# Optimization experiments

Hardware: AMD Instinct MI355X
Metric: run time of the kernel (lower is better)

## Reference

```python
import jax, jax.numpy as jnp
import numpy as np

T, B, I, H, L = 512, 32, 1024, 1024, 2


def setup_inputs() -> dict:
    key = jax.random.key(0)
    ks = jax.random.split(key, 10)
    stdv = 1.0 / np.sqrt(H)
    u = lambda k, shape: jax.random.uniform(k, shape, jnp.float32, -stdv, stdv)
    return {
        "x": jax.random.normal(ks[0], (T, B, I), jnp.float32),
        "h0": jnp.zeros((L, B, H), jnp.float32),
        "c0": jnp.zeros((L, B, H), jnp.float32),
        "W0": u(ks[1], (4 * H, I)),
        "R0": u(ks[2], (4 * H, H)),
        "bi0": u(ks[3], (4 * H,)),
        "bh0": u(ks[4], (4 * H,)),
        "W1": u(ks[5], (4 * H, H)),
        "R1": u(ks[6], (4 * H, H)),
        "bi1": u(ks[7], (4 * H,)),
        "bh1": u(ks[8], (4 * H,)),
    }


def _run_layer(x, h_init, c_init, W, R, bi, bh):
    # Precompute input projection for all timesteps: [T, B, 4H]
    xg = jnp.einsum('tbi,gi->tbg', x, W) + bi

    def step(carry, xg_t):
        h, c = carry
        gates = jax.nn.sigmoid(xg_t + h @ R.T + bh)  # [B, 4H]
        i_g, o_g, z_g, f_g = jnp.split(gates, 4, axis=-1)
        c = c * f_g + z_g - i_g          # subtractive cell update
        h = jax.nn.sigmoid(c) - o_g      # subtractive output
        return (h, c), h

    (hT, cT), out = jax.lax.scan(step, (h_init, c_init), xg)
    return out, hT, cT


def reference(x, h0, c0, W0, R0, bi0, bh0, W1, R1, bi1, bh1):
    layers = [(W0, R0, bi0, bh0), (W1, R1, bi1, bh1)]
    out = x
    h_finals, c_finals = [], []
    for l, (W, R, bi, bh) in enumerate(layers):
        out, hT, cT = _run_layer(out, h0[l], c0[l], W, R, bi, bh)
        h_finals.append(hT)
        c_finals.append(cT)
    return out, (jnp.stack(h_finals), jnp.stack(c_finals))
```

## Files before the change

### kernel.cpp

```cpp
#include <hip/hip_runtime.h>

typedef unsigned short ushort_t;
typedef unsigned int uint_t;
typedef __bf16 bf16x8 __attribute__((ext_vector_type(8)));
typedef float f32x4 __attribute__((ext_vector_type(4)));

#define T_STEPS 512
#define NWG 256

union bfu { uint4 u; bf16x8 v; };

__device__ __forceinline__ float bf2f(ushort_t u) {
  union { unsigned u; float f; } v; v.u = ((unsigned)u) << 16; return v.f;
}
__device__ __forceinline__ ushort_t f2bf(float f) {
  union { float f; unsigned u; } v; v.f = f;
  unsigned r = (v.u + 0x7FFFu + ((v.u >> 16) & 1u)) >> 16;
  return (ushort_t)r;
}
__device__ __forceinline__ uint_t pack2(float a, float b) {
  return (uint_t)f2bf(a) | ((uint_t)f2bf(b) << 16);
}
__device__ __forceinline__ float sigf(float x) {
  return 1.0f / (1.0f + __expf(-x));
}

__global__ void __launch_bounds__(256) cvt_f32_bf16(
    const float* __restrict__ in, ushort_t* __restrict__ outp, int n4) {
  int i = blockIdx.x * 256 + threadIdx.x;
  const int stride = gridDim.x * 256;
  for (; i < n4; i += stride) {
    float4 v = ((const float4*)in)[i];
    ushort4 o;
    o.x = f2bf(v.x); o.y = f2bf(v.y); o.z = f2bf(v.z); o.w = f2bf(v.w);
    ((ushort4*)outp)[i] = o;
  }
}

__global__ void __launch_bounds__(256) init_h(
    const float* __restrict__ h0_all, ushort_t* __restrict__ hpp0,
    ushort_t* __restrict__ hpp1) {
  int i = blockIdx.x * 256 + threadIdx.x;
  int l = i >> 13, j = i & 8191;
  float4 v = ((const float4*)(h0_all + l * 32768))[j];
  ushort4 o;
  o.x = f2bf(v.x); o.y = f2bf(v.y); o.z = f2bf(v.z); o.w = f2bf(v.w);
  ((ushort4*)((l ? hpp1 : hpp0) + 32768))[j] = o;
}

__global__ void __launch_bounds__(256, 1) gemm_xg(
    const float* __restrict__ X, const ushort_t* __restrict__ Wm,
    const float* __restrict__ bi, ushort_t* __restrict__ outp) {
  __shared__ char smem[65536];
  const int tid = threadIdx.x;
  const int lane = tid & 63, w = tid >> 6;
  const int m0 = blockIdx.x * 128, n0 = blockIdx.y * 128;
  const int wr = w >> 1, wc = w & 1;
  const int lr = lane & 15, kg = lane >> 4;
  const int ar_ = tid & 127;
  const int abq = (tid >> 7) * 4;

  f32x4 acc[4][4] = {};
  float4 fa[8];

  auto stageA_issue = [&](int kt) {
    const float* src = X + (size_t)(m0 + ar_) * 1024 + kt * 64 + abq * 8;
#pragma unroll
    for (int i = 0; i < 4; ++i) {
      fa[2 * i] = *(const float4*)(src + i * 8);
      fa[2 * i + 1] = *(const float4*)(src + i * 8 + 4);
    }
  };
  auto stageA_write = [&](int p) {
    char* sA = smem + p * 32768;
#pragma unroll
    for (int i = 0; i < 4; ++i) {
      int blk = abq + i;
      uint4 o;
      o.x = pack2(fa[2 * i].x, fa[2 * i].y);
      o.y = pack2(fa[2 * i].z, fa[2 * i].w);
      o.z = pack2(fa[2 * i + 1].x, fa[2 * i + 1].y);
      o.w = pack2(fa[2 * i + 1].z, fa[2 * i + 1].w);
      *(uint4*)(sA + ar_ * 128 + ((blk ^ (ar_ & 7)) << 4)) = o;
    }
  };
  auto stageB = [&](int kt, int p) {
    const int ks = kt * 64;
    char* sB = smem + p * 32768 + 16384;
#pragma unroll
    for (int i = 0; i < 4; ++i) {
      int wi = w * 4 + i;
      int e = wi * 64 + lane;
      int row = e >> 3, pb = e & 7;
      int kb = pb ^ (row & 7);
      const ushort_t* gB = Wm + (size_t)(n0 + row) * 1024 + ks + kb * 8;
      __builtin_amdgcn_global_load_lds(
          (const __attribute__((address_space(1))) void*)gB,
          (__attribute__((address_space(3))) void*)(sB + wi * 1024), 16, 0, 0);
    }
  };

  stageA_issue(0);
  stageB(0, 0);
  stageA_write(0);
  __syncthreads();
#pragma unroll 1
  for (int kt = 0; kt < 16; ++kt) {
    const int p = kt & 1;
    if (kt < 15) { stageA_issue(kt + 1); stageB(kt + 1, p ^ 1); }
    const char* sA = smem + p * 32768;
    const char* sB = sA + 16384;
#pragma unroll
    for (int k2 = 0; k2 < 2; ++k2) {
      bf16x8 af[4], bf[4];
#pragma unroll
      for (int mt = 0; mt < 4; ++mt) {
        int ar = wr * 64 + mt * 16 + lr;
        int kb = k2 * 4 + kg;
        af[mt] = *(const bf16x8*)(sA + ar * 128 + ((kb ^ (ar & 7)) << 4));
      }
#pragma unroll
      for (int nt = 0; nt < 4; ++nt) {
        int br = wc * 64 + nt * 16 + lr;
        int kb = k2 * 4 + kg;
        bf[nt] = *(const bf16x8*)(sB + br * 128 + ((kb ^ (br & 7)) << 4));
      }
#pragma unroll
      for (int mt = 0; mt < 4; ++mt)
#pragma unroll
        for (int nt = 0; nt < 4; ++nt)
          acc[mt][nt] = __builtin_amdgcn_mfma_f32_16x16x32_bf16(
              af[mt], bf[nt], acc[mt][nt], 0, 0, 0);
    }
    if (kt < 15) stageA_write(p ^ 1);
    __syncthreads();
  }
#pragma unroll
  for (int nt = 0; nt < 4; ++nt) {
    int gc = n0 + wc * 64 + nt * 16 + lr;
    int pc = ((gc & 1023) >> 3) * 32 + (gc & 7) * 4 + (gc >> 10);
    float bv = bi[gc];
#pragma unroll
    for (int mt = 0; mt < 4; ++mt) {
#pragma unroll
      for (int r = 0; r < 4; ++r) {
        int gr = m0 + wr * 64 + mt * 16 + kg * 4 + r;
        outp[(size_t)gr * 4096 + pc] = f2bf(acc[mt][nt][r] + bv);
      }
    }
  }
}

#define GLD4(dst, addr)                                        \
  asm volatile("global_load_dwordx4 %0, %1, off sc0 sc1"      \
               : "=v"(dst) : "v"(addr))
#define WAITN(N)                                               \
  do {                                                         \
    asm volatile("s_waitcnt vmcnt(" #N ")" ::: "memory");      \
    __builtin_amdgcn_sched_barrier(0);                         \
  } while (0)

__global__ void __launch_bounds__(512, 1) fused_rec(
    const ushort_t* __restrict__ xg0p, const float* __restrict__ R0,
    const float* __restrict__ R1, const float* __restrict__ W1,
    const float* __restrict__ bh0, const float* __restrict__ bi1,
    const float* __restrict__ bh1, const float* __restrict__ c0_all,
    float* __restrict__ out_f, float* __restrict__ hfinb,
    float* __restrict__ cfinb, ushort_t* __restrict__ hpp0,
    ushort_t* __restrict__ hpp1, uint_t* __restrict__ flags) {
  extern __shared__ char smem[];
  char* hl = smem;
  float* gl = (float*)(smem + 131072);

  const int tid = threadIdx.x;
  const int wg = blockIdx.x;
  const int layer = wg >> 7;
  const int wgl = wg & 127;
  const int j0 = wgl * 8;
  const int lane = tid & 63, w = tid >> 6;
  const int n16 = (w & 1) << 4;
  const int kq = w >> 1;
  const int lr16 = lane & 15, kg = lane >> 4;
  const int b = (tid >> 3) & 31, jj = tid & 7;
  const int rx = lr16 & 7;

  const int c = n16 + lr16;
  const int r_w = ((c >> 3) << 10) + j0 + (c & 7);
  bf16x8 breg[16];
  if (layer == 0) {
#pragma unroll
    for (int i = 0; i < 8; ++i) {
      const float* src = R0 + (size_t)r_w * 1024 + kq * 256 + i * 32 + kg * 8;
      float4 f0 = *(const float4*)src;
      float4 f1 = *(const float4*)(src + 4);
      bfu o;
      o.u.x = pack2(f0.x, f0.y); o.u.y = pack2(f0.z, f0.w);
      o.u.z = pack2(f1.x, f1.y); o.u.w = pack2(f1.z, f1.w);
      breg[i] = o.v;
    }
  } else {
#pragma unroll
    for (int i = 0; i < 16; ++i) {
      int k = kq * 512 + i * 32 + kg * 8;
      const float* src = (k < 1024) ? (R1 + (size_t)r_w * 1024 + k)
                                    : (W1 + (size_t)r_w * 1024 + (k - 1024));
      float4 f0 = *(const float4*)src;
      float4 f1 = *(const float4*)(src + 4);
      bfu o;
      o.u.x = pack2(f0.x, f0.y); o.u.y = pack2(f0.z, f0.w);
      o.u.z = pack2(f1.x, f1.y); o.u.w = pack2(f1.z, f1.w);
      breg[i] = o.v;
    }
  }

  float bhv[4];
#pragma unroll
  for (int g = 0; g < 4; ++g) {
    int gi = g * 1024 + j0 + jj;
    bhv[g] = layer ? (bi1[gi] + bh1[gi]) : bh0[gi];
  }
  const int cidx = b * 1024 + j0 + jj;
  float c_st = c0_all[layer * 32768 + cidx];
  uint_t* hppd = (uint_t*)(layer ? hpp1 : hpp0);
  __syncthreads();

#pragma unroll 1
  for (int s = 0; s <= T_STEPS; ++s) {
    const bool active = layer ? (s >= 1) : (s < T_STEPS);
    if (active) {
      const int t = layer ? (s - 1) : s;
      uint2 xgu = {0, 0};
      uint4 hv[16];
      if (layer == 0) {
        const char* xga = (const char*)xg0p +
            (((size_t)t * 32 + b) * 4096 + wgl * 32 + jj * 4) * 2;
        asm volatile("global_load_dwordx2 %0, %1, off"
                     : "=v"(xgu) : "v"(xga));
        const char* hsrc =
            (const char*)hpp0 + (((t + 1) & 1) << 16) + tid * 16;
#pragma unroll
        for (int l = 0; l < 8; ++l) GLD4(hv[l], hsrc + l * 8192);
        WAITN(0);
#pragma unroll
        for (int l = 0; l < 8; ++l) {
          int idx = l * 512 + tid;
          int row = idx >> 7, kb = idx & 127;
          *(uint4*)(hl + row * 2048 + ((kb ^ (row & 7)) << 4)) = hv[l];
        }
      } else {
        const char* h1src =
            (const char*)hpp1 + (((t + 1) & 1) << 16) + tid * 16;
        const char* h0src =
            (const char*)hpp0 + ((t & 1) << 16) + tid * 16;
#pragma unroll
        for (int l = 0; l < 8; ++l) GLD4(hv[l], h1src + l * 8192);
#pragma unroll
        for (int l = 0; l < 8; ++l) GLD4(hv[8 + l], h0src + l * 8192);
        WAITN(8);
#pragma unroll
        for (int l = 0; l < 8; ++l) {
          int idx = l * 512 + tid;
          int row = idx >> 7, kb = idx & 127;
          *(uint4*)(hl + row * 2048 + ((kb ^ (row & 7)) << 4)) = hv[l];
        }
        WAITN(0);
#pragma unroll
        for (int l = 0; l < 8; ++l) {
          int idx = l * 512 + tid;
          int row = idx >> 7, kb = idx & 127;
          *(uint4*)(hl + 65536 + row * 2048 + ((kb ^ (row & 7)) << 4)) =
              hv[8 + l];
        }
      }
      __syncthreads();

      f32x4 acc0 = {0.f, 0.f, 0.f, 0.f}, acc1 = {0.f, 0.f, 0.f, 0.f};
      if (layer == 0) {
        const char* a0 = hl + lr16 * 2048;
        const char* a1 = hl + (16 + lr16) * 2048;
#pragma unroll
        for (int i = 0; i < 8; ++i) {
          int kb = kq * 32 + i * 4 + kg;
          bf16x8 av0 = *(const bf16x8*)(a0 + ((kb ^ rx) << 4));
          bf16x8 av1 = *(const bf16x8*)(a1 + ((kb ^ rx) << 4));
          acc0 = __builtin_amdgcn_mfma_f32_16x16x32_bf16(av0, breg[i], acc0,
                                                         0, 0, 0);
          acc1 = __builtin_amdgcn_mfma_f32_16x16x32_bf16(av1, breg[i], acc1,
                                                         0, 0, 0);
        }
      } else {
        const char* buf = hl + ((kq >> 1) ? 65536 : 0);
        const char* a0 = buf + lr16 * 2048;
        const char* a1 = buf + (16 + lr16) * 2048;
#pragma unroll
        for (int i = 0; i < 16; ++i) {
          int kb = (kq & 1) * 64 + i * 4 + kg;
          bf16x8 av0 = *(const bf16x8*)(a0 + ((kb ^ rx) << 4));
          bf16x8 av1 = *(const bf16x8*)(a1 + ((kb ^ rx) << 4));
          acc0 = __builtin_amdgcn_mfma_f32_16x16x32_bf16(av0, breg[i], acc0,
                                                         0, 0, 0);
          acc1 = __builtin_amdgcn_mfma_f32_16x16x32_bf16(av1, breg[i], acc1,
                                                         0, 0, 0);
        }
      }
#pragma unroll
      for (int r = 0; r < 4; ++r) {
        gl[(kq * 32 + kg * 4 + r) * 33 + n16 + lr16] = acc0[r];
        gl[(kq * 32 + 16 + kg * 4 + r) * 33 + n16 + lr16] = acc1[r];
      }
      __syncthreads();

      if (tid < 256) {
        float pre[4];
#pragma unroll
        for (int g = 0; g < 4; ++g) {
          int col = g * 8 + jj;
          pre[g] = gl[(0 * 32 + b) * 33 + col] + gl[(1 * 32 + b) * 33 + col] +
                   gl[(2 * 32 + b) * 33 + col] + gl[(3 * 32 + b) * 33 + col] +
                   bhv[g];
        }
        if (layer == 0) {
          pre[0] += bf2f((ushort_t)(xgu.x & 0xffff));
          pre[1] += bf2f((ushort_t)(xgu.x >> 16));
          pre[2] += bf2f((ushort_t)(xgu.y & 0xffff));
          pre[3] += bf2f((ushort_t)(xgu.y >> 16));
        }
        float ig = sigf(pre[0]), og = sigf(pre[1]);
        float zg = sigf(pre[2]), fg = sigf(pre[3]);
        c_st = c_st * fg + zg - ig;
        float hv_ = sigf(c_st) - og;
        if (layer) out_f[(size_t)t * 32768 + cidx] = hv_;

        ushort_t hb = f2bf(hv_);
        int partner = __shfl_down((int)hb, 1, 64);
        if ((tid & 1) == 0) {
          uint_t packed =
              (uint_t)hb | (((uint_t)(unsigned short)partner) << 16);
          uint_t* dst = hppd + (((t & 1) << 14) + (cidx >> 1));
          asm volatile("global_store_dword %0, %1, off sc0 sc1"
                       :: "v"(dst), "v"(packed) : "memory");
        }
        if (t == T_STEPS - 1) {
          hfinb[layer * 32768 + cidx] = hv_;
          cfinb[layer * 32768 + cidx] = c_st;
        }
      }
    }
    if (s < T_STEPS) {
      const uint_t gen1 = (uint_t)s + 1u;
      asm volatile("s_waitcnt vmcnt(0)" ::: "memory");
      __syncthreads();
      if (tid == 0)
        __hip_atomic_store(&flags[wg], gen1, __ATOMIC_RELAXED,
                           __HIP_MEMORY_SCOPE_AGENT);
      if (tid < NWG) {
        while (__hip_atomic_load(&flags[tid], __ATOMIC_RELAXED,
                                 __HIP_MEMORY_SCOPE_AGENT) < gen1) {
          __builtin_amdgcn_s_sleep(1);
        }
      }
      __syncthreads();
      asm volatile("" ::: "memory");
    }
  }
}

extern "C" void kernel_launch(void* const* d_in, const int* in_sizes, int n_in,
                              void* d_out, int out_size, void* d_ws,
                              size_t ws_size, hipStream_t stream) {
  (void)in_sizes; (void)n_in; (void)out_size; (void)ws_size;
  const float* x = (const float*)d_in[0];
  const float* h0 = (const float*)d_in[1];
  const float* c0 = (const float*)d_in[2];
  const float* W0 = (const float*)d_in[3];
  const float* R0 = (const float*)d_in[4];
  const float* bi0 = (const float*)d_in[5];
  const float* bh0 = (const float*)d_in[6];
  const float* W1 = (const float*)d_in[7];
  const float* R1 = (const float*)d_in[8];
  const float* bi1 = (const float*)d_in[9];
  const float* bh1 = (const float*)d_in[10];
  float* outp = (float*)d_out;

  char* ws = (char*)d_ws;
  ushort_t* Wbf0 = (ushort_t*)ws;
  ushort_t* xg0p = (ushort_t*)(ws + 8388608);
  ushort_t* hpp0 = (ushort_t*)(ws + 8388608 + 134217728);
  ushort_t* hpp1 = (ushort_t*)((char*)hpp0 + 131072);
  uint_t* flags = (uint_t*)((char*)hpp1 + 131072);

  const int REC_LDS = 131072 + 4 * 32 * 33 * 4;
  (void)hipFuncSetAttribute((const void*)fused_rec,
                            hipFuncAttributeMaxDynamicSharedMemorySize,
                            REC_LDS);
  (void)hipMemsetAsync(flags, 0, NWG * sizeof(uint_t), stream);

  float* hfinb = outp + 16777216;
  float* cfinb = hfinb + 65536;

  cvt_f32_bf16<<<dim3(1024), dim3(256), 0, stream>>>(W0, Wbf0, 1048576);
  init_h<<<dim3(64), dim3(256), 0, stream>>>(h0, hpp0, hpp1);
  gemm_xg<<<dim3(128, 32), dim3(256), 0, stream>>>(x, Wbf0, bi0, xg0p);
  fused_rec<<<dim3(NWG), dim3(512), REC_LDS, stream>>>(
      xg0p, R0, R1, W1, bh0, bi1, bh1, c0, outp, hfinb, cfinb,
      hpp0, hpp1, flags);
}
```

Baseline: 4.598 ms.

## Replace global all-WG barrier with per-layer flag waits and 4-deep h0 ring

Swaps the single grid-wide barrier per step for split flags: each layer waits on its own 128 workgroups for the current step and on the other layer only for the dependency it needs. Layer 1 waits for layer 0 step t, and layer 0 may run up to three steps ahead of layer 1. To allow that slack, layer 0's hidden-state buffer becomes a 4-slot ring and the xg load is prefetched one step ahead. This removes lockstep coupling between the layers and the cross-layer skew wait, at the cost of more complex ring indexing and more memory-ordering risk.

```diff
diff --git a/kernel.cpp b/kernel.cpp
--- a/kernel.cpp
+++ b/kernel.cpp
@@ -45,7 +45,7 @@
   float4 v = ((const float4*)(h0_all + l * 32768))[j];
   ushort4 o;
   o.x = f2bf(v.x); o.y = f2bf(v.y); o.z = f2bf(v.z); o.w = f2bf(v.w);
-  ((ushort4*)((l ? hpp1 : hpp0) + 32768))[j] = o;
+  ((ushort4*)(l ? (hpp1 + 32768) : (hpp0 + 98304)))[j] = o;
 }
 
 __global__ void __launch_bounds__(256, 1) gemm_xg(
@@ -167,7 +167,8 @@
     const float* __restrict__ bh1, const float* __restrict__ c0_all,
     float* __restrict__ out_f, float* __restrict__ hfinb,
     float* __restrict__ cfinb, ushort_t* __restrict__ hpp0,
-    ushort_t* __restrict__ hpp1, uint_t* __restrict__ flags) {
+    ushort_t* __restrict__ hpp1, uint_t* __restrict__ flags0,
+    uint_t* __restrict__ flags1) {
   extern __shared__ char smem[];
   char* hl = smem;
   float* gl = (float*)(smem + 131072);
@@ -184,6 +185,9 @@
   const int b = (tid >> 3) & 31, jj = tid & 7;
   const int rx = lr16 & 7;
 
+  uint_t* fown = layer ? flags1 : flags0;
+  uint_t* foth = layer ? flags0 : flags1;
+
   const int c = n16 + lr16;
   const int r_w = ((c >> 3) << 10) + j0 + (c & 7);
   bf16x8 breg[16];
@@ -222,146 +226,154 @@
   const int cidx = b * 1024 + j0 + jj;
   float c_st = c0_all[layer * 32768 + cidx];
   uint_t* hppd = (uint_t*)(layer ? hpp1 : hpp0);
+
+  const char* xgbase = (const char*)xg0p +
+      ((size_t)b * 4096 + (size_t)wgl * 32 + (size_t)jj * 4) * 2;
+  uint2 xgu = {0, 0}, xgn = {0, 0};
+  if (layer == 0)
+    asm volatile("global_load_dwordx2 %0, %1, off" : "=v"(xgu) : "v"(xgbase));
   __syncthreads();
 
 #pragma unroll 1
-  for (int s = 0; s <= T_STEPS; ++s) {
-    const bool active = layer ? (s >= 1) : (s < T_STEPS);
-    if (active) {
-      const int t = layer ? (s - 1) : s;
-      uint2 xgu = {0, 0};
-      uint4 hv[16];
-      if (layer == 0) {
-        const char* xga = (const char*)xg0p +
-            (((size_t)t * 32 + b) * 4096 + wgl * 32 + jj * 4) * 2;
-        asm volatile("global_load_dwordx2 %0, %1, off"
-                     : "=v"(xgu) : "v"(xga));
-        const char* hsrc =
-            (const char*)hpp0 + (((t + 1) & 1) << 16) + tid * 16;
-#pragma unroll
-        for (int l = 0; l < 8; ++l) GLD4(hv[l], hsrc + l * 8192);
-        WAITN(0);
-#pragma unroll
-        for (int l = 0; l < 8; ++l) {
-          int idx = l * 512 + tid;
-          int row = idx >> 7, kb = idx & 127;
-          *(uint4*)(hl + row * 2048 + ((kb ^ (row & 7)) << 4)) = hv[l];
-        }
-      } else {
-        const char* h1src =
-            (const char*)hpp1 + (((t + 1) & 1) << 16) + tid * 16;
-        const char* h0src =
-            (const char*)hpp0 + ((t & 1) << 16) + tid * 16;
-#pragma unroll
-        for (int l = 0; l < 8; ++l) GLD4(hv[l], h1src + l * 8192);
-#pragma unroll
-        for (int l = 0; l < 8; ++l) GLD4(hv[8 + l], h0src + l * 8192);
-        WAITN(8);
-#pragma unroll
-        for (int l = 0; l < 8; ++l) {
-          int idx = l * 512 + tid;
-          int row = idx >> 7, kb = idx & 127;
-          *(uint4*)(hl + row * 2048 + ((kb ^ (row & 7)) << 4)) = hv[l];
-        }
-        WAITN(0);
-#pragma unroll
-        for (int l = 0; l < 8; ++l) {
-          int idx = l * 512 + tid;
-          int row = idx >> 7, kb = idx & 127;
-          *(uint4*)(hl + 65536 + row * 2048 + ((kb ^ (row & 7)) << 4)) =
-              hv[8 + l];
-        }
-      }
-      __syncthreads();
-
-      f32x4 acc0 = {0.f, 0.f, 0.f, 0.f}, acc1 = {0.f, 0.f, 0.f, 0.f};
-      if (layer == 0) {
-        const char* a0 = hl + lr16 * 2048;
-        const char* a1 = hl + (16 + lr16) * 2048;
-#pragma unroll
-        for (int i = 0; i < 8; ++i) {
-          int kb = kq * 32 + i * 4 + kg;
-          bf16x8 av0 = *(const bf16x8*)(a0 + ((kb ^ rx) << 4));
-          bf16x8 av1 = *(const bf16x8*)(a1 + ((kb ^ rx) << 4));
-          acc0 = __builtin_amdgcn_mfma_f32_16x16x32_bf16(av0, breg[i], acc0,
-                                                         0, 0, 0);
-          acc1 = __builtin_amdgcn_mfma_f32_16x16x32_bf16(av1, breg[i], acc1,
-                                                         0, 0, 0);
-        }
-      } else {
-        const char* buf = hl + ((kq >> 1) ? 65536 : 0);
-        const char* a0 = buf + lr16 * 2048;
-        const char* a1 = buf + (16 + lr16) * 2048;
-#pragma unroll
-        for (int i = 0; i < 16; ++i) {
-          int kb = (kq & 1) * 64 + i * 4 + kg;
-          bf16x8 av0 = *(const bf16x8*)(a0 + ((kb ^ rx) << 4));
-          bf16x8 av1 = *(const bf16x8*)(a1 + ((kb ^ rx) << 4));
-          acc0 = __builtin_amdgcn_mfma_f32_16x16x32_bf16(av0, breg[i], acc0,
-                                                         0, 0, 0);
-          acc1 = __builtin_amdgcn_mfma_f32_16x16x32_bf16(av1, breg[i], acc1,
-                                                         0, 0, 0);
-        }
-      }
-#pragma unroll
-      for (int r = 0; r < 4; ++r) {
-        gl[(kq * 32 + kg * 4 + r) * 33 + n16 + lr16] = acc0[r];
-        gl[(kq * 32 + 16 + kg * 4 + r) * 33 + n16 + lr16] = acc1[r];
-      }
-      __syncthreads();
-
-      if (tid < 256) {
-        float pre[4];
-#pragma unroll
-        for (int g = 0; g < 4; ++g) {
-          int col = g * 8 + jj;
-          pre[g] = gl[(0 * 32 + b) * 33 + col] + gl[(1 * 32 + b) * 33 + col] +
-                   gl[(2 * 32 + b) * 33 + col] + gl[(3 * 32 + b) * 33 + col] +
-                   bhv[g];
-        }
-        if (layer == 0) {
-          pre[0] += bf2f((ushort_t)(xgu.x & 0xffff));
-          pre[1] += bf2f((ushort_t)(xgu.x >> 16));
-          pre[2] += bf2f((ushort_t)(xgu.y & 0xffff));
-          pre[3] += bf2f((ushort_t)(xgu.y >> 16));
-        }
-        float ig = sigf(pre[0]), og = sigf(pre[1]);
-        float zg = sigf(pre[2]), fg = sigf(pre[3]);
-        c_st = c_st * fg + zg - ig;
-        float hv_ = sigf(c_st) - og;
-        if (layer) out_f[(size_t)t * 32768 + cidx] = hv_;
-
-        ushort_t hb = f2bf(hv_);
-        int partner = __shfl_down((int)hb, 1, 64);
-        if ((tid & 1) == 0) {
-          uint_t packed =
-              (uint_t)hb | (((uint_t)(unsigned short)partner) << 16);
-          uint_t* dst = hppd + (((t & 1) << 14) + (cidx >> 1));
-          asm volatile("global_store_dword %0, %1, off sc0 sc1"
-                       :: "v"(dst), "v"(packed) : "memory");
-        }
-        if (t == T_STEPS - 1) {
-          hfinb[layer * 32768 + cidx] = hv_;
-          cfinb[layer * 32768 + cidx] = c_st;
-        }
-      }
-    }
-    if (s < T_STEPS) {
-      const uint_t gen1 = (uint_t)s + 1u;
-      asm volatile("s_waitcnt vmcnt(0)" ::: "memory");
-      __syncthreads();
-      if (tid == 0)
-        __hip_atomic_store(&flags[wg], gen1, __ATOMIC_RELAXED,
-                           __HIP_MEMORY_SCOPE_AGENT);
-      if (tid < NWG) {
-        while (__hip_atomic_load(&flags[tid], __ATOMIC_RELAXED,
-                                 __HIP_MEMORY_SCOPE_AGENT) < gen1) {
+  for (int t = 0; t < T_STEPS; ++t) {
+    {
+      const int genOwn = t;
+      const int genOth = layer ? (t + 1) : (t - 3);
+      if (tid < 128) {
+        while ((int)__hip_atomic_load(&fown[tid], __ATOMIC_RELAXED,
+                                      __HIP_MEMORY_SCOPE_AGENT) < genOwn)
           __builtin_amdgcn_s_sleep(1);
-        }
+      } else if (tid < 256) {
+        while ((int)__hip_atomic_load(&foth[tid - 128], __ATOMIC_RELAXED,
+                                      __HIP_MEMORY_SCOPE_AGENT) < genOth)
+          __builtin_amdgcn_s_sleep(1);
       }
       __syncthreads();
       asm volatile("" ::: "memory");
     }
+
+    uint4 hv[16];
+    if (layer == 0) {
+      if (t + 1 < T_STEPS)
+        asm volatile("global_load_dwordx2 %0, %1, off"
+                     : "=v"(xgn) : "v"(xgbase + (size_t)(t + 1) * 262144));
+      const char* hsrc =
+          (const char*)hpp0 + (((t + 3) & 3) << 16) + tid * 16;
+#pragma unroll
+      for (int l = 0; l < 8; ++l) GLD4(hv[l], hsrc + l * 8192);
+      WAITN(0);
+#pragma unroll
+      for (int l = 0; l < 8; ++l) {
+        int idx = l * 512 + tid;
+        int row = idx >> 7, kb = idx & 127;
+        *(uint4*)(hl + row * 2048 + ((kb ^ (row & 7)) << 4)) = hv[l];
+      }
+    } else {
+      const char* h1src =
+          (const char*)hpp1 + (((t + 1) & 1) << 16) + tid * 16;
+      const char* h0src =
+          (const char*)hpp0 + ((t & 3) << 16) + tid * 16;
+#pragma unroll
+      for (int l = 0; l < 8; ++l) GLD4(hv[l], h1src + l * 8192);
+#pragma unroll
+      for (int l = 0; l < 8; ++l) GLD4(hv[8 + l], h0src + l * 8192);
+      WAITN(8);
+#pragma unroll
+      for (int l = 0; l < 8; ++l) {
+        int idx = l * 512 + tid;
+        int row = idx >> 7, kb = idx & 127;
+        *(uint4*)(hl + row * 2048 + ((kb ^ (row & 7)) << 4)) = hv[l];
+      }
+      WAITN(0);
+#pragma unroll
+      for (int l = 0; l < 8; ++l) {
+        int idx = l * 512 + tid;
+        int row = idx >> 7, kb = idx & 127;
+        *(uint4*)(hl + 65536 + row * 2048 + ((kb ^ (row & 7)) << 4)) =
+            hv[8 + l];
+      }
+    }
+    __syncthreads();
+
+    f32x4 acc0 = {0.f, 0.f, 0.f, 0.f}, acc1 = {0.f, 0.f, 0.f, 0.f};
+    if (layer == 0) {
+      const char* a0 = hl + lr16 * 2048;
+      const char* a1 = hl + (16 + lr16) * 2048;
+#pragma unroll
+      for (int i = 0; i < 8; ++i) {
+        int kb = kq * 32 + i * 4 + kg;
+        bf16x8 av0 = *(const bf16x8*)(a0 + ((kb ^ rx) << 4));
+        bf16x8 av1 = *(const bf16x8*)(a1 + ((kb ^ rx) << 4));
+        acc0 = __builtin_amdgcn_mfma_f32_16x16x32_bf16(av0, breg[i], acc0,
+                                                       0, 0, 0);
+        acc1 = __builtin_amdgcn_mfma_f32_16x16x32_bf16(av1, breg[i], acc1,
+                                                       0, 0, 0);
+      }
+    } else {
+      const char* buf = hl + ((kq >> 1) ? 65536 : 0);
+      const char* a0 = buf + lr16 * 2048;
+      const char* a1 = buf + (16 + lr16) * 2048;
+#pragma unroll
+      for (int i = 0; i < 16; ++i) {
+        int kb = (kq & 1) * 64 + i * 4 + kg;
+        bf16x8 av0 = *(const bf16x8*)(a0 + ((kb ^ rx) << 4));
+        bf16x8 av1 = *(const bf16x8*)(a1 + ((kb ^ rx) << 4));
+        acc0 = __builtin_amdgcn_mfma_f32_16x16x32_bf16(av0, breg[i], acc0,
+                                                       0, 0, 0);
+        acc1 = __builtin_amdgcn_mfma_f32_16x16x32_bf16(av1, breg[i], acc1,
+                                                       0, 0, 0);
+      }
+    }
+#pragma unroll
+    for (int r = 0; r < 4; ++r) {
+      gl[(kq * 32 + kg * 4 + r) * 33 + n16 + lr16] = acc0[r];
+      gl[(kq * 32 + 16 + kg * 4 + r) * 33 + n16 + lr16] = acc1[r];
+    }
+    __syncthreads();
+
+    if (tid < 256) {
+      float pre[4];
+#pragma unroll
+      for (int g = 0; g < 4; ++g) {
+        int col = g * 8 + jj;
+        pre[g] = gl[(0 * 32 + b) * 33 + col] + gl[(1 * 32 + b) * 33 + col] +
+                 gl[(2 * 32 + b) * 33 + col] + gl[(3 * 32 + b) * 33 + col] +
+                 bhv[g];
+      }
+      if (layer == 0) {
+        pre[0] += bf2f((ushort_t)(xgu.x & 0xffff));
+        pre[1] += bf2f((ushort_t)(xgu.x >> 16));
+        pre[2] += bf2f((ushort_t)(xgu.y & 0xffff));
+        pre[3] += bf2f((ushort_t)(xgu.y >> 16));
+      }
+      float ig = sigf(pre[0]), og = sigf(pre[1]);
+      float zg = sigf(pre[2]), fg = sigf(pre[3]);
+      c_st = c_st * fg + zg - ig;
+      float hv_ = sigf(c_st) - og;
+      if (layer) out_f[(size_t)t * 32768 + cidx] = hv_;
+
+      ushort_t hb = f2bf(hv_);
+      int partner = __shfl_down((int)hb, 1, 64);
+      if ((tid & 1) == 0) {
+        uint_t packed =
+            (uint_t)hb | (((uint_t)(unsigned short)partner) << 16);
+        uint_t* dst = hppd +
+            ((layer ? ((t & 1) << 14) : ((t & 3) << 14)) + (cidx >> 1));
+        asm volatile("global_store_dword %0, %1, off sc0 sc1"
+                     :: "v"(dst), "v"(packed) : "memory");
+      }
+      if (t == T_STEPS - 1) {
+        hfinb[layer * 32768 + cidx] = hv_;
+        cfinb[layer * 32768 + cidx] = c_st;
+      }
+    }
+
+    asm volatile("s_waitcnt vmcnt(0)" ::: "memory");
+    __syncthreads();
+    if (tid == 0)
+      __hip_atomic_store(&fown[wgl], (uint_t)(t + 1), __ATOMIC_RELAXED,
+                         __HIP_MEMORY_SCOPE_AGENT);
+    if (layer == 0) xgu = xgn;
   }
 }
 
@@ -386,14 +398,15 @@
   ushort_t* Wbf0 = (ushort_t*)ws;
   ushort_t* xg0p = (ushort_t*)(ws + 8388608);
   ushort_t* hpp0 = (ushort_t*)(ws + 8388608 + 134217728);
-  ushort_t* hpp1 = (ushort_t*)((char*)hpp0 + 131072);
-  uint_t* flags = (uint_t*)((char*)hpp1 + 131072);
+  ushort_t* hpp1 = (ushort_t*)((char*)hpp0 + 262144);
+  uint_t* flags0 = (uint_t*)((char*)hpp1 + 131072);
+  uint_t* flags1 = flags0 + 128;
 
   const int REC_LDS = 131072 + 4 * 32 * 33 * 4;
   (void)hipFuncSetAttribute((const void*)fused_rec,
                             hipFuncAttributeMaxDynamicSharedMemorySize,
                             REC_LDS);
-  (void)hipMemsetAsync(flags, 0, NWG * sizeof(uint_t), stream);
+  (void)hipMemsetAsync(flags0, 0, 256 * sizeof(uint_t), stream);
 
   float* hfinb = outp + 16777216;
   float* cfinb = hfinb + 65536;
@@ -403,5 +416,5 @@
   gemm_xg<<<dim3(128, 32), dim3(256), 0, stream>>>(x, Wbf0, bi0, xg0p);
   fused_rec<<<dim3(NWG), dim3(512), REC_LDS, stream>>>(
       xg0p, R0, R1, W1, bh0, bi1, bh1, c0, outp, hfinb, cfinb,
-      hpp0, hpp1, flags);
-}
+      hpp0, hpp1, flags0, flags1);
+}
```

Measured after the change: 4.425 ms. 3.8% less time.
